# Performance work log

Measured on AMD Instinct MI355X. Metric: run time of the kernel, lower is better.

The kernel has to match this reference:

```python
import jax, jax.numpy as jnp
import numpy as np

B, N, S = 64, 128, 100          # batch, pod_num, seq_len
E, H, M = 64, 128, 3            # embed_dim, hidden_dim, modal_num
VOCAB = 2000
FIN = M * S * (E + 1)           # shared_encoder in_features = 19500
FG = M * H                      # gat feature dim = 384
MAX_EVENT_LEN = 100.0
LEAKY_ALPHA = 0.2


def setup_inputs() -> dict:
    key = jax.random.key(0)
    ks = jax.random.split(key, 16)
    inp = {
        "l_e": jax.random.randint(ks[0], (B, N, S), 0, VOCAB),
        "m_e": jax.random.randint(ks[1], (B, N, S), 0, VOCAB),
        "t_e": jax.random.randint(ks[2], (B, N, S), 0, VOCAB),
        "l_c": jax.random.uniform(ks[3], (B, N, S), jnp.float32) * 100.0,
        "m_c": jax.random.uniform(ks[4], (B, N, S), jnp.float32) * 100.0,
        "t_c": jax.random.uniform(ks[5], (B, N, S), jnp.float32) * 100.0,
        "adj": (jax.random.uniform(ks[6], (N, N)) > 0.5).astype(jnp.float32),
        # learned parameters (weights stored as (in, out); y = x @ W + b)
        "emb": jax.random.normal(ks[7], (VOCAB, E), jnp.float32) * 0.02,
        "W_se": jax.random.normal(ks[8], (FIN, 3 * H), jnp.float32) * (1.0 / np.sqrt(FIN)),
        "b_se": jnp.zeros((3 * H,), jnp.float32),
        "gat_W": jax.random.normal(ks[9], (FG, FG), jnp.float32) * (1.0 / np.sqrt(FG)),
        "gat_a": jax.random.normal(ks[10], (2 * FG, 1), jnp.float32) * 0.1,
        "W1": jax.random.normal(ks[11], (FG * N, N), jnp.float32) * (1.0 / np.sqrt(FG * N)),
        "b1": jnp.zeros((N,), jnp.float32),
    }
    return inp


def gat_layer(x, adj, W, a):
    """Faithful GraphAttentionLayer (concat=True, dropout=0) without materializing
    the [B,N,N,2F] a_input: e_ij = leakyrelu(a1.h_i + a2.h_j)."""
    h = x @ W                                      # [B,N,F]
    F_ = W.shape[1]
    a1, a2 = a[:F_, 0], a[F_:, 0]
    e = jax.nn.leaky_relu(
        (h @ a1)[:, :, None] + (h @ a2)[:, None, :], LEAKY_ALPHA
    )                                              # [B,N,N]
    att = jnp.where(adj > 0, e, -1e12)
    att = jax.nn.softmax(att, axis=-1)
    return jax.nn.relu(att @ h)                    # [B,N,F]


def reference(l_e, m_e, t_e, l_c, m_c, t_c, adj, emb, W_se, b_se, gat_W, gat_a, W1, b1):
    # embedding lookup + concat normalized event counts -> [B,N,S,E+1] per modality
    log_r = jnp.concatenate([emb[l_e], (l_c / MAX_EVENT_LEN)[..., None]], -1)
    metric_r = jnp.concatenate([emb[m_e], (m_c / MAX_EVENT_LEN)[..., None]], -1)
    trace_r = jnp.concatenate([emb[t_e], (t_c / MAX_EVENT_LEN)[..., None]], -1)
    # shared encoder: cat on feature dim, flatten per node, dense -> [B,N,3H]
    fused = jnp.concatenate([log_r, metric_r, trace_r], -1).reshape(B, N, -1)
    fusion_r = fused @ W_se + b_se
    # GAT + residual + linear head (use_gat_linear path)
    out = gat_layer(fusion_r, adj, gat_W, gat_a)
    x = fusion_r + out
    x = x.reshape(B, -1) @ W1 + b1                 # [B,N]
    return (x, fusion_r)
```

## Files before the change

kernel.cpp:

```cpp
#include <hip/hip_runtime.h>

#define KB_TOT 305
#define KPAD   19520
#define BROW   39040

typedef __attribute__((ext_vector_type(8))) short bf16x8_t;
typedef __attribute__((ext_vector_type(4))) float f32x4_t;

typedef const __attribute__((address_space(1))) unsigned int GAS_u32;
typedef __attribute__((address_space(3))) unsigned int LAS_u32;

__device__ inline unsigned short f2bf(float x) {
    union { float f; unsigned u; } a; a.f = x;
    unsigned r = a.u + 0x7fffu + ((a.u >> 16) & 1u);
    return (unsigned short)(r >> 16);
}
__device__ inline float bf2f(unsigned short h) {
    union { unsigned u; float f; } a; a.u = ((unsigned)h) << 16; return a.f;
}
__device__ inline unsigned long long pack4bf(float x, float y, float z, float w) {
    return (unsigned long long)f2bf(x) | ((unsigned long long)f2bf(y) << 16)
         | ((unsigned long long)f2bf(z) << 32) | ((unsigned long long)f2bf(w) << 48);
}

__global__ __launch_bounds__(256) void prep_kernel(
    const float* __restrict__ emb, const float* __restrict__ l_c,
    const float* __restrict__ m_c, const float* __restrict__ t_c,
    const float* __restrict__ W_se, const float* __restrict__ gat_W,
    const float* __restrict__ W1,
    unsigned short* __restrict__ ebf, unsigned short* __restrict__ Ac,
    unsigned short* __restrict__ WT, unsigned short* __restrict__ Bws,
    unsigned short* __restrict__ W1T) {
    __shared__ float tl[64 * 68];
    int bid = blockIdx.x, tid = threadIdx.x;
    if (bid < 125) {
        int i4 = (bid * 256 + tid) * 4;
        float4 v = *(const float4*)(emb + i4);
        *(unsigned long long*)(ebf + i4) = pack4bf(v.x, v.y, v.z, v.w);
    } else if (bid < 2685) {
        int lin = (bid - 125) * 256 + tid;
        int row = lin / 80, c4 = (lin - row * 80) * 4;
        float vv[4];
        #pragma unroll
        for (int ii = 0; ii < 4; ++ii) {
            int t = c4 + ii;
            float x = 0.f;
            if (t < 300) {
                int m = t / 100, s = t - m * 100;
                const float* C = (m == 0) ? l_c : ((m == 1) ? m_c : t_c);
                x = C[row * 100 + s] * 0.01f;
            }
            vv[ii] = x;
        }
        *(unsigned long long*)(Ac + row * 320 + c4) = pack4bf(vv[0], vv[1], vv[2], vv[3]);
    } else if (bid < 2721) {
        int idx = bid - 2685;
        int k0 = (idx % 6) * 64, n0 = (idx / 6) * 64;
        int rr = tid >> 2, c16 = (tid & 3) * 16;
        #pragma unroll
        for (int ii = 0; ii < 4; ++ii)
            *(float4*)(tl + rr * 68 + c16 + ii * 4) =
                *(const float4*)(gat_W + (k0 + rr) * 384 + n0 + c16 + ii * 4);
        __syncthreads();
        int c = tid >> 2, r16 = (tid & 3) * 16;
        unsigned long long* dst8 = (unsigned long long*)(WT + (n0 + c) * 384 + k0 + r16);
        #pragma unroll
        for (int q = 0; q < 4; ++q) {
            int rb = r16 + q * 4;
            dst8[q] = pack4bf(tl[(rb + 0) * 68 + c], tl[(rb + 1) * 68 + c],
                              tl[(rb + 2) * 68 + c], tl[(rb + 3) * 68 + c]);
        }
    } else if (bid < 4551) {
        int idx = bid - 2721;
        int kb = idx % 305, h0 = (idx / 305) * 64;
        int rr = tid >> 2, c16 = (tid & 3) * 16;
        float4 v[4];
        if (kb < 300) {
            int m = kb / 100, s = kb - m * 100;
            const float* srcp = W_se + (s * 195 + m * 65 + rr) * 384 + h0 + c16;
            #pragma unroll
            for (int ii = 0; ii < 4; ++ii) v[ii] = *(const float4*)(srcp + ii * 4);
        } else {
            int t = (kb - 300) * 64 + rr;
            if (t < 300) {
                int m = t / 100, s = t - m * 100;
                const float* srcp = W_se + (s * 195 + m * 65 + 64) * 384 + h0 + c16;
                #pragma unroll
                for (int ii = 0; ii < 4; ++ii) v[ii] = *(const float4*)(srcp + ii * 4);
            } else {
                #pragma unroll
                for (int ii = 0; ii < 4; ++ii) v[ii] = make_float4(0.f, 0.f, 0.f, 0.f);
            }
        }
        #pragma unroll
        for (int ii = 0; ii < 4; ++ii) *(float4*)(tl + rr * 68 + c16 + ii * 4) = v[ii];
        __syncthreads();
        int c = tid >> 2, r16 = (tid & 3) * 16;
        unsigned long long* dst8 =
            (unsigned long long*)(Bws + (unsigned)(h0 + c) * KPAD + kb * 64 + r16);
        #pragma unroll
        for (int q = 0; q < 4; ++q) {
            int rb = r16 + q * 4;
            dst8[q] = pack4bf(tl[(rb + 0) * 68 + c], tl[(rb + 1) * 68 + c],
                              tl[(rb + 2) * 68 + c], tl[(rb + 3) * 68 + c]);
        }
    } else {
        int idx = bid - 4551;
        int k0 = (idx % 768) * 64, n0 = (idx / 768) * 64;
        int rr = tid >> 2, c16 = (tid & 3) * 16;
        #pragma unroll
        for (int ii = 0; ii < 4; ++ii)
            *(float4*)(tl + rr * 68 + c16 + ii * 4) =
                *(const float4*)(W1 + (size_t)(k0 + rr) * 128 + n0 + c16 + ii * 4);
        __syncthreads();
        int c = tid >> 2, r16 = (tid & 3) * 16;
        unsigned long long* dst8 =
            (unsigned long long*)(W1T + (size_t)(n0 + c) * 49152 + k0 + r16);
        #pragma unroll
        for (int q = 0; q < 4; ++q) {
            int rb = r16 + q * 4;
            dst8[q] = pack4bf(tl[(rb + 0) * 68 + c], tl[(rb + 1) * 68 + c],
                              tl[(rb + 2) * 68 + c], tl[(rb + 3) * 68 + c]);
        }
    }
}

__global__ __launch_bounds__(256) void gemm_fused_kernel(
    const int* __restrict__ l_e, const int* __restrict__ m_e, const int* __restrict__ t_e,
    const unsigned short* __restrict__ emb_bf, const unsigned short* __restrict__ Ac_bf,
    const unsigned short* __restrict__ Bws, float* __restrict__ fusion_d,
    unsigned short* __restrict__ Pbf) {

    __shared__ alignas(16) unsigned short Al[128 * 64];
    __shared__ alignas(16) unsigned short Bl[128 * 64];

    const int tid  = threadIdx.x;
    const int lane = tid & 63;
    const int wid  = tid >> 6;

    int bid = blockIdx.x;
    int lin = (bid & 7) * 96 + (bid >> 3);
    const int mt = lin % 64;
    int rest = lin / 64;
    const int nt = rest % 3;
    const int kc = rest / 3;
    const int bm0 = mt * 128;
    const int h0  = nt * 128;
    int kb        = (kc == 0) ? 0 : (77 + (kc - 1) * 76);
    const int kbe = 77 + kc * 76 > KB_TOT ? KB_TOT : 77 + kc * 76;

    const int l7 = lane & 7, l3 = lane >> 3;
    const int voffA = ((l7 ^ l3) << 4);
    const int rowg0 = bm0 + wid * 32 + l3;

    f32x4_t acc[4][4];
    #pragma unroll
    for (int i = 0; i < 4; ++i)
        #pragma unroll
        for (int j = 0; j < 4; ++j) acc[i][j] = (f32x4_t){0.f, 0.f, 0.f, 0.f};

    const int wr = wid >> 1, wc = wid & 1;
    const int l15 = lane & 15, l4 = lane >> 4;

    int idx4[4];
    if (kb < 300) {
        int m = kb / 100, s = kb - m * 100;
        const int* I = (m == 0) ? l_e : ((m == 1) ? m_e : t_e);
        const int* Ib = I + rowg0 * 100 + s;
        idx4[0] = Ib[0]; idx4[1] = Ib[800]; idx4[2] = Ib[1600]; idx4[3] = Ib[2400];
    }

    for (; kb < kbe; ++kb) {
        if (kb < 300) {
            #pragma unroll
            for (int p = 0; p < 4; ++p) {
                const char* src = (const char*)emb_bf + ((long)idx4[p] << 7) + voffA;
                __builtin_amdgcn_global_load_lds((GAS_u32*)src,
                    (LAS_u32*)((char*)Al + (wid * 4 + p) * 1024), 16, 0, 0);
            }
        } else {
            int q = kb - 300;
            #pragma unroll
            for (int p = 0; p < 4; ++p) {
                const char* src = (const char*)Ac_bf + (long)(rowg0 + p * 8) * 640
                                + q * 128 + voffA;
                __builtin_amdgcn_global_load_lds((GAS_u32*)src,
                    (LAS_u32*)((char*)Al + (wid * 4 + p) * 1024), 16, 0, 0);
            }
        }
        #pragma unroll
        for (int p = 0; p < 4; ++p) {
            int ch = wid * 4 + p;
            int hl = ch * 8 + l3;
            long gb = (long)(h0 + hl) * BROW + kb * 128 + ((l7 << 4) ^ (l3 << 4));
            __builtin_amdgcn_global_load_lds((GAS_u32*)((const char*)Bws + gb),
                                             (LAS_u32*)((char*)Bl + ch * 1024), 16, 0, 0);
        }
        int kn = kb + 1;
        if (kn < 300 && kn < kbe) {
            int m = kn / 100, s = kn - m * 100;
            const int* I = (m == 0) ? l_e : ((m == 1) ? m_e : t_e);
            const int* Ib = I + rowg0 * 100 + s;
            idx4[0] = Ib[0]; idx4[1] = Ib[800]; idx4[2] = Ib[1600]; idx4[3] = Ib[2400];
        }
        __syncthreads();
        #pragma unroll
        for (int ks = 0; ks < 2; ++ks) {
            int kb2 = ks * 64 + l4 * 16;
            bf16x8_t af[4], bfr[4];
            #pragma unroll
            for (int i = 0; i < 4; ++i) {
                int row = wr * 64 + i * 16 + l15;
                af[i]  = *(const bf16x8_t*)((const char*)Al + row * 128 + (kb2 ^ ((row & 7) << 4)));
                int col = wc * 64 + i * 16 + l15;
                bfr[i] = *(const bf16x8_t*)((const char*)Bl + col * 128 + (kb2 ^ ((col & 7) << 4)));
            }
            #pragma unroll
            for (int i = 0; i < 4; ++i)
                #pragma unroll
                for (int j = 0; j < 4; ++j)
                    acc[i][j] = __builtin_amdgcn_mfma_f32_16x16x32_bf16(af[i], bfr[j], acc[i][j], 0, 0, 0);
        }
        __syncthreads();
    }
    if (kc == 0) {
        #pragma unroll
        for (int i = 0; i < 4; ++i)
            #pragma unroll
            for (int j = 0; j < 4; ++j)
                #pragma unroll
                for (int r = 0; r < 4; ++r) {
                    int row = bm0 + wr * 64 + i * 16 + l4 * 4 + r;
                    int col = h0 + wc * 64 + j * 16 + l15;
                    fusion_d[row * 384 + col] = acc[i][j][r];
                }
    } else {
        unsigned short* dst = Pbf + (size_t)(kc - 1) * 3145728;
        #pragma unroll
        for (int i = 0; i < 4; ++i)
            #pragma unroll
            for (int j = 0; j < 4; ++j)
                #pragma unroll
                for (int r = 0; r < 4; ++r) {
                    int row = bm0 + wr * 64 + i * 16 + l4 * 4 + r;
                    int col = h0 + wc * 64 + j * 16 + l15;
                    dst[row * 384 + col] = f2bf(acc[i][j][r]);
                }
    }
}

__global__ __launch_bounds__(256) void reduce_fusion_kernel(float* __restrict__ fusion_d,
                                                            const unsigned short* __restrict__ Pbf,
                                                            const float* __restrict__ b_se,
                                                            unsigned short* __restrict__ fusion_bf,
                                                            float* __restrict__ e_ws) {
    if (blockIdx.x < 16) {
        int z = blockIdx.x * 1024 + threadIdx.x * 4;
        *(float4*)(e_ws + z) = make_float4(0.f, 0.f, 0.f, 0.f);
    }
    int i4 = blockIdx.x * 256 + threadIdx.x;
    int col4 = (i4 % 96) * 4;
    float4 a = *(const float4*)(fusion_d + i4 * 4);
    float4 bs = *(const float4*)(b_se + col4);
    float s0 = a.x + bs.x, s1 = a.y + bs.y, s2 = a.z + bs.z, s3 = a.w + bs.w;
    #pragma unroll
    for (int sl = 0; sl < 3; ++sl) {
        ushort4 p = *(const ushort4*)(Pbf + (size_t)sl * 3145728 + i4 * 4);
        s0 += bf2f(p.x); s1 += bf2f(p.y); s2 += bf2f(p.z); s3 += bf2f(p.w);
    }
    *(float4*)(fusion_d + i4 * 4) = make_float4(s0, s1, s2, s3);
    *(unsigned long long*)(fusion_bf + i4 * 4) = pack4bf(s0, s1, s2, s3);
}

__global__ __launch_bounds__(256) void gat_h_kernel(const unsigned short* __restrict__ fusion_bf,
                                                    const unsigned short* __restrict__ WT,
                                                    const float* __restrict__ gat_a,
                                                    unsigned short* __restrict__ hT,
                                                    float* __restrict__ e_ws) {
    __shared__ alignas(16) unsigned short Al[128 * 64];
    __shared__ alignas(16) unsigned short Bl[128 * 64];
    const int tid  = threadIdx.x;
    const int lane = tid & 63;
    const int wid  = tid >> 6;
    const int b  = blockIdx.x;
    const int c0 = blockIdx.y * 128;
    const int l7 = lane & 7, l3 = lane >> 3;
    const int voffA = ((l7 ^ l3) << 4);
    const int wr = wid >> 1, wc = wid & 1;
    const int l15 = lane & 15, l4 = lane >> 4;

    f32x4_t acc[4][4];
    #pragma unroll
    for (int i = 0; i < 4; ++i)
        #pragma unroll
        for (int j = 0; j < 4; ++j) acc[i][j] = (f32x4_t){0.f, 0.f, 0.f, 0.f};

    for (int kb = 0; kb < 6; ++kb) {
        #pragma unroll
        for (int p = 0; p < 4; ++p) {
            int ch = wid * 4 + p;
            int rl = ch * 8 + l3;
            long ga = (long)(b * 128 + rl) * 768 + kb * 128 + voffA;
            __builtin_amdgcn_global_load_lds((GAS_u32*)((const char*)fusion_bf + ga),
                                             (LAS_u32*)((char*)Al + ch * 1024), 16, 0, 0);
            long gb = (long)(c0 + rl) * 768 + kb * 128 + voffA;
            __builtin_amdgcn_global_load_lds((GAS_u32*)((const char*)WT + gb),
                                             (LAS_u32*)((char*)Bl + ch * 1024), 16, 0, 0);
        }
        __syncthreads();
        #pragma unroll
        for (int ks = 0; ks < 2; ++ks) {
            int kb2 = ks * 64 + l4 * 16;
            bf16x8_t af[4], bfr[4];
            #pragma unroll
            for (int i = 0; i < 4; ++i) {
                int row = wr * 64 + i * 16 + l15;
                af[i]  = *(const bf16x8_t*)((const char*)Al + row * 128 + (kb2 ^ ((row & 7) << 4)));
                int col = wc * 64 + i * 16 + l15;
                bfr[i] = *(const bf16x8_t*)((const char*)Bl + col * 128 + (kb2 ^ ((col & 7) << 4)));
            }
            #pragma unroll
            for (int i = 0; i < 4; ++i)
                #pragma unroll
                for (int j = 0; j < 4; ++j)
                    acc[i][j] = __builtin_amdgcn_mfma_f32_16x16x32_bf16(af[i], bfr[j], acc[i][j], 0, 0, 0);
        }
        __syncthreads();
    }
    #pragma unroll
    for (int i = 0; i < 4; ++i)
        #pragma unroll
        for (int j = 0; j < 4; ++j) {
            int nb = wr * 64 + i * 16 + l4 * 4;
            int f  = c0 + wc * 64 + j * 16 + l15;
            *(unsigned long long*)(hT + ((size_t)(b * 384 + f)) * 128 + nb) =
                pack4bf(acc[i][j][0], acc[i][j][1], acc[i][j][2], acc[i][j][3]);
        }
    float a1v[4], a2v[4];
    #pragma unroll
    for (int j = 0; j < 4; ++j) {
        int f = c0 + wc * 64 + j * 16 + l15;
        a1v[j] = gat_a[f];
        a2v[j] = gat_a[384 + f];
    }
    #pragma unroll
    for (int i = 0; i < 4; ++i)
        #pragma unroll
        for (int r = 0; r < 4; ++r) {
            float p1 = 0.f, p2 = 0.f;
            #pragma unroll
            for (int j = 0; j < 4; ++j) {
                float hv = acc[i][j][r];
                p1 += hv * a1v[j];
                p2 += hv * a2v[j];
            }
            #pragma unroll
            for (int m = 1; m < 16; m <<= 1) {
                p1 += __shfl_xor(p1, m);
                p2 += __shfl_xor(p2, m);
            }
            if (l15 == 0) {
                int n = wr * 64 + i * 16 + l4 * 4 + r;
                atomicAdd(&e_ws[b * 128 + n], p1);
                atomicAdd(&e_ws[8192 + b * 128 + n], p2);
            }
        }
}

__global__ __launch_bounds__(256) void gat_pv_kernel(const float* __restrict__ e_ws,
                                                     const float* __restrict__ adj,
                                                     const unsigned short* __restrict__ hT,
                                                     const float* __restrict__ fusion_d,
                                                     unsigned short* __restrict__ x_pre_bf) {
    __shared__ alignas(16) unsigned short Pl[128 * 128];
    __shared__ alignas(16) unsigned short Bl[128 * 128];
    __shared__ float se2[128];
    const int tid  = threadIdx.x;
    const int lane = tid & 63;
    const int wid  = tid >> 6;
    const int b  = blockIdx.x;
    const int f0 = blockIdx.y * 128;
    const int wr = wid >> 1, wc = wid & 1;
    const int l15 = lane & 15, l4 = lane >> 4;

    if (tid < 128) se2[tid] = e_ws[8192 + b * 128 + tid];
    #pragma unroll
    for (int p = 0; p < 8; ++p) {
        int ch = wid * 8 + p;
        int row = ch * 4 + (lane >> 4);
        long gb = (long)(b * 384 + f0 + row) * 256 + (((lane & 15) ^ (row & 7)) << 4);
        __builtin_amdgcn_global_load_lds((GAS_u32*)((const char*)hT + gb),
                                         (LAS_u32*)((char*)Bl + ch * 1024), 16, 0, 0);
    }
    __syncthreads();

    {
        int r = tid >> 1, half = tid & 1;
        float er = e_ws[b * 128 + r];
        const float* arow = adj + r * 128 + half * 64;
        const float* e2h = se2 + half * 64;
        float mx = -1e30f;
        #pragma unroll 8
        for (int j = 0; j < 64; ++j) {
            float v = er + e2h[j];
            v = (v > 0.f) ? v : 0.2f * v;
            v = (arow[j] > 0.f) ? v : -1e12f;
            mx = fmaxf(mx, v);
        }
        mx = fmaxf(mx, __shfl_xor(mx, 1));
        float sum = 0.f;
        #pragma unroll 8
        for (int j = 0; j < 64; ++j) {
            float v = er + e2h[j];
            v = (v > 0.f) ? v : 0.2f * v;
            v = (arow[j] > 0.f) ? v : -1e12f;
            sum += __expf(v - mx);
        }
        sum += __shfl_xor(sum, 1);
        float inv = 1.f / sum;
        #pragma unroll
        for (int g = 0; g < 8; ++g) {
            float vv[8];
            #pragma unroll
            for (int q = 0; q < 8; ++q) {
                int j = g * 8 + q;
                float v = er + e2h[j];
                v = (v > 0.f) ? v : 0.2f * v;
                v = (arow[j] > 0.f) ? v : -1e12f;
                vv[q] = __expf(v - mx) * inv;
            }
            char* dst = (char*)Pl + r * 256 + ((half * 128 + g * 16) ^ ((r & 7) << 4));
            *(unsigned long long*)dst       = pack4bf(vv[0], vv[1], vv[2], vv[3]);
            *(unsigned long long*)(dst + 8) = pack4bf(vv[4], vv[5], vv[6], vv[7]);
        }
    }
    __syncthreads();

    f32x4_t acc[4][4];
    #pragma unroll
    for (int i = 0; i < 4; ++i)
        #pragma unroll
        for (int j = 0; j < 4; ++j) acc[i][j] = (f32x4_t){0.f, 0.f, 0.f, 0.f};

    #pragma unroll
    for (int st = 0; st < 4; ++st) {
        int ko = st * 64 + l4 * 16;
        bf16x8_t af[4], bfr[4];
        #pragma unroll
        for (int i = 0; i < 4; ++i) {
            int row = wr * 64 + i * 16 + l15;
            af[i]  = *(const bf16x8_t*)((const char*)Pl + row * 256 + (ko ^ ((row & 7) << 4)));
            int col = wc * 64 + i * 16 + l15;
            bfr[i] = *(const bf16x8_t*)((const char*)Bl + col * 256 + (ko ^ ((col & 7) << 4)));
        }
        #pragma unroll
        for (int i = 0; i < 4; ++i)
            #pragma unroll
            for (int j = 0; j < 4; ++j)
                acc[i][j] = __builtin_amdgcn_mfma_f32_16x16x32_bf16(af[i], bfr[j], acc[i][j], 0, 0, 0);
    }
    #pragma unroll
    for (int i = 0; i < 4; ++i)
        #pragma unroll
        for (int j = 0; j < 4; ++j) {
            int f = f0 + wc * 64 + j * 16 + l15;
            #pragma unroll
            for (int r = 0; r < 4; ++r) {
                int n = wr * 64 + i * 16 + l4 * 4 + r;
                float v = acc[i][j][r];
                v = (v > 0.f ? v : 0.f) + fusion_d[(b * 128 + n) * 384 + f];
                x_pre_bf[(size_t)b * 49152 + n * 384 + f] = f2bf(v);
            }
        }
}

__global__ __launch_bounds__(256) void final_kernel(const unsigned short* __restrict__ x_pre_bf,
                                                    const unsigned short* __restrict__ W1T,
                                                    float* __restrict__ pf) {
    __shared__ alignas(16) unsigned short Al[64 * 64];
    __shared__ alignas(16) unsigned short Bl[128 * 64];
    const int tid  = threadIdx.x;
    const int lane = tid & 63;
    const int wid  = tid >> 6;
    const int kc   = blockIdx.x;
    const int l7 = lane & 7, l3 = lane >> 3;
    const int voffA = ((l7 ^ l3) << 4);
    const int l15 = lane & 15, l4 = lane >> 4;

    f32x4_t acc[4][2];
    #pragma unroll
    for (int i = 0; i < 4; ++i) {
        acc[i][0] = (f32x4_t){0.f, 0.f, 0.f, 0.f};
        acc[i][1] = (f32x4_t){0.f, 0.f, 0.f, 0.f};
    }

    for (int ks = 0; ks < 3; ++ks) {
        #pragma unroll
        for (int p = 0; p < 2; ++p) {
            int ch = wid * 2 + p;
            int row = ch * 8 + l3;
            long ga = (long)row * 98304 + kc * 384 + ks * 128 + voffA;
            __builtin_amdgcn_global_load_lds((GAS_u32*)((const char*)x_pre_bf + ga),
                                             (LAS_u32*)((char*)Al + ch * 1024), 16, 0, 0);
        }
        #pragma unroll
        for (int p = 0; p < 4; ++p) {
            int ch = wid * 4 + p;
            int col = ch * 8 + l3;
            long gb = (long)col * 98304 + kc * 384 + ks * 128 + voffA;
            __builtin_amdgcn_global_load_lds((GAS_u32*)((const char*)W1T + gb),
                                             (LAS_u32*)((char*)Bl + ch * 1024), 16, 0, 0);
        }
        __syncthreads();
        #pragma unroll
        for (int ks2 = 0; ks2 < 2; ++ks2) {
            int kb2 = ks2 * 64 + l4 * 16;
            bf16x8_t af[4], bfr[2];
            #pragma unroll
            for (int i = 0; i < 4; ++i) {
                int row = i * 16 + l15;
                af[i] = *(const bf16x8_t*)((const char*)Al + row * 128 + (kb2 ^ ((row & 7) << 4)));
            }
            #pragma unroll
            for (int j = 0; j < 2; ++j) {
                int col = wid * 32 + j * 16 + l15;
                bfr[j] = *(const bf16x8_t*)((const char*)Bl + col * 128 + (kb2 ^ ((col & 7) << 4)));
            }
            #pragma unroll
            for (int i = 0; i < 4; ++i) {
                acc[i][0] = __builtin_amdgcn_mfma_f32_16x16x32_bf16(af[i], bfr[0], acc[i][0], 0, 0, 0);
                acc[i][1] = __builtin_amdgcn_mfma_f32_16x16x32_bf16(af[i], bfr[1], acc[i][1], 0, 0, 0);
            }
        }
        __syncthreads();
    }
    float* dst = pf + (size_t)kc * 8192;
    #pragma unroll
    for (int i = 0; i < 4; ++i)
        #pragma unroll
        for (int j = 0; j < 2; ++j) {
            int col = wid * 32 + j * 16 + l15;
            #pragma unroll
            for (int r = 0; r < 4; ++r) {
                int row = i * 16 + l4 * 4 + r;
                dst[row * 128 + col] = acc[i][j][r];
            }
        }
}

__global__ __launch_bounds__(256) void reduce_final_kernel(const float* __restrict__ pf,
                                                           const float* __restrict__ b1,
                                                           float* __restrict__ xout) {
    int i = blockIdx.x * 256 + threadIdx.x;
    float acc = 0.f;
    #pragma unroll 8
    for (int s = 0; s < 256; ++s) acc += pf[(size_t)s * 8192 + i];
    xout[i] = acc + b1[i & 127];
}

extern "C" void kernel_launch(void* const* d_in, const int* in_sizes, int n_in,
                              void* d_out, int out_size, void* d_ws, size_t ws_size,
                              hipStream_t stream) {
    (void)in_sizes; (void)n_in; (void)out_size; (void)ws_size;
    const int*   l_e   = (const int*)d_in[0];
    const int*   m_e   = (const int*)d_in[1];
    const int*   t_e   = (const int*)d_in[2];
    const float* l_c   = (const float*)d_in[3];
    const float* m_c   = (const float*)d_in[4];
    const float* t_c   = (const float*)d_in[5];
    const float* adj   = (const float*)d_in[6];
    const float* emb   = (const float*)d_in[7];
    const float* W_se  = (const float*)d_in[8];
    const float* b_se  = (const float*)d_in[9];
    const float* gat_W = (const float*)d_in[10];
    const float* gat_a = (const float*)d_in[11];
    const float* W1    = (const float*)d_in[12];
    const float* b1    = (const float*)d_in[13];

    float* xout     = (float*)d_out;
    float* fusion_d = xout + 8192;

    char* ws = (char*)d_ws;
    unsigned short* Bws    = (unsigned short*)(ws);
    unsigned short* emb_bf = (unsigned short*)(ws + 15728640);
    unsigned short* Ac_bf  = (unsigned short*)(ws + 15990784);
    unsigned short* WT_bf  = (unsigned short*)(ws + 21233664);
    unsigned short* Pbf    = (unsigned short*)(ws + 21528576);
    unsigned short* W1T_bf = (unsigned short*)(ws + 40402944);
    unsigned short* fusion_bf = (unsigned short*)(ws);
    unsigned short* hT_bf     = (unsigned short*)(ws + 6291456);
    unsigned short* x_pre_bf  = (unsigned short*)(ws + 12582912);
    float*          e_ws      = (float*)(ws + 18874368);
    float*          pf        = (float*)(ws + 21528576);

    prep_kernel<<<6087, 256, 0, stream>>>(emb, l_c, m_c, t_c, W_se, gat_W, W1,
                                          emb_bf, Ac_bf, WT_bf, Bws, W1T_bf);
    gemm_fused_kernel<<<768, 256, 0, stream>>>(l_e, m_e, t_e, emb_bf, Ac_bf, Bws, fusion_d, Pbf);
    reduce_fusion_kernel<<<3072, 256, 0, stream>>>(fusion_d, Pbf, b_se, fusion_bf, e_ws);
    gat_h_kernel<<<dim3(64, 3), 256, 0, stream>>>(fusion_bf, WT_bf, gat_a, hT_bf, e_ws);
    gat_pv_kernel<<<dim3(64, 3), 256, 0, stream>>>(e_ws, adj, hT_bf, fusion_d, x_pre_bf);
    final_kernel<<<256, 256, 0, stream>>>(x_pre_bf, W1T_bf, pf);
    reduce_final_kernel<<<32, 256, 0, stream>>>(pf, b1, xout);
}
```

Baseline: 319.9 us.

## Double-buffer LDS tiles in fused GEMM with manual vmcnt waits

Converts the single-buffered LDS A/B tiles of the shared-encoder GEMM into a two-stage ping-pong pipeline. The next k-block's global-to-LDS loads and the embedding index loads two steps ahead are issued before computing on the current buffer, with explicit s_waitcnt vmcnt counts and raw s_barrier in place of __syncthreads. The aim is to hide global/gather latency behind MFMA work. It doubles LDS use to 64 KB per block, which may reduce occupancy, and relies on hand-tuned waitcnt values being correct.

```diff
diff --git a/kernel.cpp b/kernel.cpp
--- a/kernel.cpp
+++ b/kernel.cpp
@@ -131,8 +131,8 @@
     const unsigned short* __restrict__ Bws, float* __restrict__ fusion_d,
     unsigned short* __restrict__ Pbf) {
 
-    __shared__ alignas(16) unsigned short Al[128 * 64];
-    __shared__ alignas(16) unsigned short Bl[128 * 64];
+    __shared__ alignas(16) unsigned short Al[2][128 * 64];
+    __shared__ alignas(16) unsigned short Bl[2][128 * 64];
 
     const int tid  = threadIdx.x;
     const int lane = tid & 63;
@@ -162,48 +162,68 @@
     const int wr = wid >> 1, wc = wid & 1;
     const int l15 = lane & 15, l4 = lane >> 4;
 
-    int idx4[4];
-    if (kb < 300) {
-        int m = kb / 100, s = kb - m * 100;
-        const int* I = (m == 0) ? l_e : ((m == 1) ? m_e : t_e);
-        const int* Ib = I + rowg0 * 100 + s;
-        idx4[0] = Ib[0]; idx4[1] = Ib[800]; idx4[2] = Ib[1600]; idx4[3] = Ib[2400];
-    }
-
+    int idxA[4], idxB[4];
+
+    #define LOAD_IDX(n, d) { \
+        int m_ = (n) / 100, s_ = (n) - m_ * 100; \
+        const int* I_ = (m_ == 0) ? l_e : ((m_ == 1) ? m_e : t_e); \
+        const int* Ib_ = I_ + rowg0 * 100 + s_; \
+        d[0] = Ib_[0]; d[1] = Ib_[800]; d[2] = Ib_[1600]; d[3] = Ib_[2400]; }
+
+    #define STAGE(buf, n, ix) { \
+        if ((n) < 300) { \
+            _Pragma("unroll") \
+            for (int p_ = 0; p_ < 4; ++p_) { \
+                const char* src_ = (const char*)emb_bf + ((long)ix[p_] << 7) + voffA; \
+                __builtin_amdgcn_global_load_lds((GAS_u32*)src_, \
+                    (LAS_u32*)((char*)&Al[buf][0] + (wid * 4 + p_) * 1024), 16, 0, 0); \
+            } \
+        } else { \
+            int q_ = (n) - 300; \
+            _Pragma("unroll") \
+            for (int p_ = 0; p_ < 4; ++p_) { \
+                const char* src_ = (const char*)Ac_bf + (long)(rowg0 + p_ * 8) * 640 \
+                                 + q_ * 128 + voffA; \
+                __builtin_amdgcn_global_load_lds((GAS_u32*)src_, \
+                    (LAS_u32*)((char*)&Al[buf][0] + (wid * 4 + p_) * 1024), 16, 0, 0); \
+            } \
+        } \
+        _Pragma("unroll") \
+        for (int p_ = 0; p_ < 4; ++p_) { \
+            int ch_ = wid * 4 + p_; \
+            int hl_ = ch_ * 8 + l3; \
+            long gb_ = (long)(h0 + hl_) * BROW + (n) * 128 + ((l7 << 4) ^ (l3 << 4)); \
+            __builtin_amdgcn_global_load_lds((GAS_u32*)((const char*)Bws + gb_), \
+                (LAS_u32*)((char*)&Bl[buf][0] + ch_ * 1024), 16, 0, 0); \
+        } }
+
+    if (kb < 300) LOAD_IDX(kb, idxB);
+    { int n1 = kb + 1; if (n1 < kbe && n1 < 300) LOAD_IDX(n1, idxA); }
+    STAGE(0, kb, idxB);
+
+    int cur = 0;
     for (; kb < kbe; ++kb) {
-        if (kb < 300) {
-            #pragma unroll
-            for (int p = 0; p < 4; ++p) {
-                const char* src = (const char*)emb_bf + ((long)idx4[p] << 7) + voffA;
-                __builtin_amdgcn_global_load_lds((GAS_u32*)src,
-                    (LAS_u32*)((char*)Al + (wid * 4 + p) * 1024), 16, 0, 0);
-            }
+        int nk = kb + 1;
+        if (nk < kbe) {
+            #pragma unroll
+            for (int i2 = 0; i2 < 4; ++i2) idxB[i2] = idxA[i2];
+            int nn = nk + 1;
+            bool nxidx = (nn < kbe) && (nn < 300);
+            if (nxidx) LOAD_IDX(nn, idxA);
+            STAGE(cur ^ 1, nk, idxB);
+            __builtin_amdgcn_sched_barrier(0);
+            if (nxidx) asm volatile("s_waitcnt vmcnt(12)" ::: "memory");
+            else       asm volatile("s_waitcnt vmcnt(8)"  ::: "memory");
         } else {
-            int q = kb - 300;
-            #pragma unroll
-            for (int p = 0; p < 4; ++p) {
-                const char* src = (const char*)Ac_bf + (long)(rowg0 + p * 8) * 640
-                                + q * 128 + voffA;
-                __builtin_amdgcn_global_load_lds((GAS_u32*)src,
-                    (LAS_u32*)((char*)Al + (wid * 4 + p) * 1024), 16, 0, 0);
-            }
-        }
-        #pragma unroll
-        for (int p = 0; p < 4; ++p) {
-            int ch = wid * 4 + p;
-            int hl = ch * 8 + l3;
-            long gb = (long)(h0 + hl) * BROW + kb * 128 + ((l7 << 4) ^ (l3 << 4));
-            __builtin_amdgcn_global_load_lds((GAS_u32*)((const char*)Bws + gb),
-                                             (LAS_u32*)((char*)Bl + ch * 1024), 16, 0, 0);
-        }
-        int kn = kb + 1;
-        if (kn < 300 && kn < kbe) {
-            int m = kn / 100, s = kn - m * 100;
-            const int* I = (m == 0) ? l_e : ((m == 1) ? m_e : t_e);
-            const int* Ib = I + rowg0 * 100 + s;
-            idx4[0] = Ib[0]; idx4[1] = Ib[800]; idx4[2] = Ib[1600]; idx4[3] = Ib[2400];
-        }
-        __syncthreads();
+            __builtin_amdgcn_sched_barrier(0);
+            asm volatile("s_waitcnt vmcnt(0)" ::: "memory");
+        }
+        __builtin_amdgcn_sched_barrier(0);
+        __builtin_amdgcn_s_barrier();
+        __builtin_amdgcn_sched_barrier(0);
+
+        const char* Ab = (const char*)&Al[cur][0];
+        const char* Bb = (const char*)&Bl[cur][0];
         #pragma unroll
         for (int ks = 0; ks < 2; ++ks) {
             int kb2 = ks * 64 + l4 * 16;
@@ -211,9 +231,9 @@
             #pragma unroll
             for (int i = 0; i < 4; ++i) {
                 int row = wr * 64 + i * 16 + l15;
-                af[i]  = *(const bf16x8_t*)((const char*)Al + row * 128 + (kb2 ^ ((row & 7) << 4)));
+                af[i]  = *(const bf16x8_t*)(Ab + row * 128 + (kb2 ^ ((row & 7) << 4)));
                 int col = wc * 64 + i * 16 + l15;
-                bfr[i] = *(const bf16x8_t*)((const char*)Bl + col * 128 + (kb2 ^ ((col & 7) << 4)));
+                bfr[i] = *(const bf16x8_t*)(Bb + col * 128 + (kb2 ^ ((col & 7) << 4)));
             }
             #pragma unroll
             for (int i = 0; i < 4; ++i)
@@ -221,8 +241,16 @@
                 for (int j = 0; j < 4; ++j)
                     acc[i][j] = __builtin_amdgcn_mfma_f32_16x16x32_bf16(af[i], bfr[j], acc[i][j], 0, 0, 0);
         }
-        __syncthreads();
-    }
+        __builtin_amdgcn_sched_barrier(0);
+        asm volatile("s_waitcnt lgkmcnt(0)" ::: "memory");
+        __builtin_amdgcn_sched_barrier(0);
+        __builtin_amdgcn_s_barrier();
+        __builtin_amdgcn_sched_barrier(0);
+        cur ^= 1;
+    }
+    #undef LOAD_IDX
+    #undef STAGE
+
     if (kc == 0) {
         #pragma unroll
         for (int i = 0; i < 4; ++i)
```

After: 369.9 us. 15.6% more time.
